# Optimization experiments

Hardware: AMD Instinct MI355X
Metric: run time of the kernel (lower is better)

## Reference

```python
import jax, jax.numpy as jnp
import numpy as np

N = 50000      # nodes
E = 800000     # edges (avg degree 16)
D_IN = 128     # node_feature_dim
H = 256        # hidden_dim
EPS = 1e-5     # BatchNorm eps


def setup_inputs() -> dict:
    key = jax.random.key(0)
    ks = jax.random.split(key, 32)
    inp = {
        "x": jax.random.normal(ks[0], (N, D_IN), jnp.float32),
        "edge_index": jax.random.randint(ks[1], (2, E), 0, N, jnp.int32),
    }
    dims = [(D_IN, H), (H, H), (H, H)]
    k = 2
    for i, (din, dout) in enumerate(dims):
        s = 1.0 / np.sqrt(din)
        inp[f"Wl{i}"] = jax.random.uniform(ks[k], (din, dout), jnp.float32, -s, s); k += 1
        inp[f"bl{i}"] = jax.random.uniform(ks[k], (dout,), jnp.float32, -s, s); k += 1
        inp[f"Wr{i}"] = jax.random.uniform(ks[k], (din, dout), jnp.float32, -s, s); k += 1
        inp[f"g{i}"] = jnp.ones((dout,), jnp.float32)
        inp[f"b{i}"] = jnp.zeros((dout,), jnp.float32)
        inp[f"rm{i}"] = jax.random.normal(ks[k], (dout,), jnp.float32) * 0.1; k += 1
        inp[f"rv{i}"] = jax.random.uniform(ks[k], (dout,), jnp.float32, 0.5, 1.5); k += 1
    return inp


def _sage(x, src, dst, Wl, bl, Wr):
    # PyG SAGEConv (aggr='mean'): out = lin_l(mean_{j in N(i)} x_j) + lin_r(x_i)
    deg = jax.ops.segment_sum(jnp.ones((src.shape[0],), x.dtype), dst, num_segments=N)
    agg = jax.ops.segment_sum(x[src], dst, num_segments=N)  # [N, d_in]
    mean = agg / jnp.maximum(deg, 1.0)[:, None]
    return mean @ Wl + bl + x @ Wr


def _bn(x, g, b, rm, rv):
    # eval-mode BatchNorm1d with running stats
    return (x - rm) * (g * jax.lax.rsqrt(rv + EPS)) + b


def reference(x, edge_index,
              Wl0, bl0, Wr0, g0, b0, rm0, rv0,
              Wl1, bl1, Wr1, g1, b1, rm1, rv1,
              Wl2, bl2, Wr2, g2, b2, rm2, rv2):
    src, dst = edge_index[0], edge_index[1]
    h = jax.nn.relu(_bn(_sage(x, src, dst, Wl0, bl0, Wr0), g0, b0, rm0, rv0))
    h = jax.nn.relu(_bn(_sage(h, src, dst, Wl1, bl1, Wr1), g1, b1, rm1, rv1))
    h = _bn(_sage(h, src, dst, Wl2, bl2, Wr2), g2, b2, rm2, rv2)
    return h  # [N, H] node embeddings (dropout is identity in eval mode)
```

## Files before the change

### kernel.cpp

```cpp
#include <hip/hip_runtime.h>
#include <hip/hip_bf16.h>

#define NNODES 50000
#define NEDGES 800000
#define HID 256
#define BN_EPS 1e-5f
#define SCAN_B ((NNODES + 255) / 256)

typedef __attribute__((ext_vector_type(8))) short short8v;
typedef __attribute__((ext_vector_type(4))) float f32x4;

__device__ inline void load_lds16(const void* g, void* l) {
    __builtin_amdgcn_global_load_lds(
        (const __attribute__((address_space(1))) unsigned int*)g,
        (__attribute__((address_space(3))) unsigned int*)l, 16, 0, 0);
}

__global__ void k_zero(int* p, int n) {
    int i = blockIdx.x * blockDim.x + threadIdx.x;
    if (i < n) p[i] = 0;
}

__global__ void k_countrank(const int* __restrict__ ei, int* __restrict__ cnt,
                            int* __restrict__ rank, int nE) {
    int e = blockIdx.x * blockDim.x + threadIdx.x;
    if (e < nE) rank[e] = atomicAdd(&cnt[ei[nE + e]], 1);
}

__global__ void k_bsum(const int* __restrict__ cnt, int* __restrict__ loc,
                       int* __restrict__ bsum, int n) {
    __shared__ int sh[256];
    int tid = threadIdx.x;
    int i = blockIdx.x * 256 + tid;
    int v = (i < n) ? cnt[i] : 0;
    sh[tid] = v;
    __syncthreads();
    for (int off = 1; off < 256; off <<= 1) {
        int t = (tid >= off) ? sh[tid - off] : 0;
        __syncthreads();
        sh[tid] += t;
        __syncthreads();
    }
    if (i < n) loc[i] = sh[tid] - v;
    if (tid == 255) bsum[blockIdx.x] = sh[255];
}

__global__ void k_bscan(int* __restrict__ bsum, int nb) {
    __shared__ int sh[256];
    int tid = threadIdx.x;
    int v = (tid < nb) ? bsum[tid] : 0;
    sh[tid] = v;
    __syncthreads();
    for (int off = 1; off < 256; off <<= 1) {
        int t = (tid >= off) ? sh[tid - off] : 0;
        __syncthreads();
        sh[tid] += t;
        __syncthreads();
    }
    if (tid < nb) bsum[tid] = sh[tid] - v;
}

__global__ void k_addoff(const int* __restrict__ loc, const int* __restrict__ bsum,
                         int* __restrict__ rowptr, int n, int nE) {
    int i = blockIdx.x * 256 + threadIdx.x;
    if (i < n) rowptr[i] = loc[i] + bsum[blockIdx.x];
    if (i == 0) rowptr[n] = nE;
}

__global__ void k_fill2(const int* __restrict__ ei, const int* __restrict__ rowptr,
                        const int* __restrict__ rank, int* __restrict__ col, int nE) {
    int e = blockIdx.x * blockDim.x + threadIdx.x;
    if (e < nE) col[rowptr[ei[nE + e]] + rank[e]] = ei[e];
}

__global__ void k_cast(const float* __restrict__ in, __hip_bfloat16* __restrict__ out, int n) {
    int i = blockIdx.x * blockDim.x + threadIdx.x;
    int base = i * 4;
    if (base + 3 < n) {
        float4 v = *(const float4*)(in + base);
        out[base + 0] = __float2bfloat16(v.x);
        out[base + 1] = __float2bfloat16(v.y);
        out[base + 2] = __float2bfloat16(v.z);
        out[base + 3] = __float2bfloat16(v.w);
    } else {
        for (int j = base; j < n; j++) out[j] = __float2bfloat16(in[j]);
    }
}

__global__ void k_transpose6(const float* __restrict__ s0, const float* __restrict__ s1,
                             const float* __restrict__ s2, const float* __restrict__ s3,
                             const float* __restrict__ s4, const float* __restrict__ s5,
                             __hip_bfloat16* __restrict__ d0, __hip_bfloat16* __restrict__ d1,
                             __hip_bfloat16* __restrict__ d2, __hip_bfloat16* __restrict__ d3,
                             __hip_bfloat16* __restrict__ d4, __hip_bfloat16* __restrict__ d5) {
    int f = blockIdx.x * blockDim.x + threadIdx.x;
    const float* src; __hip_bfloat16* dst; int K; int i;
    if (f < 65536) {
        K = 128;
        if (f < 32768) { src = s0; dst = d0; i = f; }
        else           { src = s1; dst = d1; i = f - 32768; }
    } else {
        K = 256;
        int r = f - 65536;
        int wsel = r >> 16;
        i = r & 65535;
        src = (wsel == 0) ? s2 : (wsel == 1) ? s3 : (wsel == 2) ? s4 : s5;
        dst = (wsel == 0) ? d2 : (wsel == 1) ? d3 : (wsel == 2) ? d4 : d5;
    }
    int k = i >> 8;
    int nn = i & 255;
    dst[nn * K + k] = __float2bfloat16(src[i]);
}

template <int D, int U>
__global__ void k_mean(const __hip_bfloat16* __restrict__ xin,
                       const int* __restrict__ rowptr, const int* __restrict__ col,
                       __hip_bfloat16* __restrict__ mean, int n) {
    constexpr int CPL = D / 8;
    constexpr int R = 64 / CPL;
    int gw = (blockIdx.x * blockDim.x + threadIdx.x) >> 6;
    int lane = threadIdx.x & 63;
    if (gw >= n) return;
    int beg = rowptr[gw], end = rowptr[gw + 1];
    int sub = lane / CPL;
    int fpos = lane % CPL;
    const uint4* base = (const uint4*)xin;

    float acc[8];
#pragma unroll
    for (int j = 0; j < 8; j++) acc[j] = 0.f;

    for (int p0 = beg; p0 < end; p0 += U * R) {
        int idx[U]; bool ok[U];
#pragma unroll
        for (int u = 0; u < U; u++) {
            int p = p0 + u * R + sub;
            ok[u] = (p < end);
            idx[u] = ok[u] ? col[p] : 0;
        }
        uint4 v[U];
#pragma unroll
        for (int u = 0; u < U; u++) {
            uint4 t = {0u, 0u, 0u, 0u};
            if (ok[u]) t = base[(size_t)idx[u] * CPL + fpos];
            v[u] = t;
        }
#pragma unroll
        for (int u = 0; u < U; u++) {
            const unsigned int uu[4] = {v[u].x, v[u].y, v[u].z, v[u].w};
#pragma unroll
            for (int j = 0; j < 4; j++) {
                acc[2 * j]     += __uint_as_float(uu[j] << 16);
                acc[2 * j + 1] += __uint_as_float(uu[j] & 0xffff0000u);
            }
        }
    }

    if constexpr (R >= 2) {
#pragma unroll
        for (int j = 0; j < 8; j++) acc[j] += __shfl_xor(acc[j], 32, 64);
    }
    if constexpr (R == 4) {
#pragma unroll
        for (int j = 0; j < 8; j++) acc[j] += __shfl_xor(acc[j], 16, 64);
    }

    if (sub == 0) {
        float inv = (end > beg) ? 1.f / (float)(end - beg) : 0.f;
        union { uint4 v; unsigned short s[8]; } o;
#pragma unroll
        for (int j = 0; j < 8; j++)
            o.s[j] = __bfloat16_as_ushort(__float2bfloat16(acc[j] * inv));
        *(uint4*)(mean + (size_t)gw * D + fpos * 8) = o.v;
    }
}

template <int K, typename OutT, int RELU>
__launch_bounds__(256)
__global__ void k_gemm(const __hip_bfloat16* __restrict__ A1,
                       const __hip_bfloat16* __restrict__ A2,
                       const __hip_bfloat16* __restrict__ W1t,
                       const __hip_bfloat16* __restrict__ W2t,
                       const float* __restrict__ bl,
                       const float* __restrict__ g,
                       const float* __restrict__ bb,
                       const float* __restrict__ rm,
                       const float* __restrict__ rv,
                       OutT* __restrict__ out, int n) {
    __shared__ __hip_bfloat16 As1[128 * 32];
    __shared__ __hip_bfloat16 As2[128 * 32];
    __shared__ __hip_bfloat16 Bs1[128 * 32];
    __shared__ __hip_bfloat16 Bs2[128 * 32];
    int tid = threadIdx.x;
    int lane = tid & 63;
    int w = tid >> 6;
    int quad = lane >> 4;
    int ml = lane & 15;
    int rowBase = (blockIdx.x >> 1) * 128;
    int colBase = (blockIdx.x & 1) * 128;
    int wr = w >> 1, wc = w & 1;

    f32x4 acc[4][4];
#pragma unroll
    for (int i = 0; i < 4; i++)
#pragma unroll
        for (int t = 0; t < 4; t++) acc[i][t] = {0.f, 0.f, 0.f, 0.f};

    int srow = tid >> 2;
    int sbyte = (tid & 3) * 16;

    for (int k0 = 0; k0 < K; k0 += 32) {
        __syncthreads();
#pragma unroll
        for (int h = 0; h < 2; h++) {
            int r = srow + h * 64;
            int grow = rowBase + r; if (grow >= n) grow = n - 1;
            int c = colBase + r;
            load_lds16((const char*)(A1 + (size_t)grow * K + k0) + sbyte,
                       (char*)As1 + r * 64 + sbyte);
            load_lds16((const char*)(A2 + (size_t)grow * K + k0) + sbyte,
                       (char*)As2 + r * 64 + sbyte);
            load_lds16((const char*)(W1t + (size_t)c * K + k0) + sbyte,
                       (char*)Bs1 + r * 64 + sbyte);
            load_lds16((const char*)(W2t + (size_t)c * K + k0) + sbyte,
                       (char*)Bs2 + r * 64 + sbyte);
        }
        __syncthreads();

        short8v af1[4], af2[4], bf1[4], bf2[4];
#pragma unroll
        for (int i = 0; i < 4; i++) {
            af1[i] = *(const short8v*)(As1 + (wr * 64 + i * 16 + ml) * 32 + quad * 8);
            af2[i] = *(const short8v*)(As2 + (wr * 64 + i * 16 + ml) * 32 + quad * 8);
        }
#pragma unroll
        for (int t = 0; t < 4; t++) {
            bf1[t] = *(const short8v*)(Bs1 + (wc * 64 + t * 16 + ml) * 32 + quad * 8);
            bf2[t] = *(const short8v*)(Bs2 + (wc * 64 + t * 16 + ml) * 32 + quad * 8);
        }
#pragma unroll
        for (int i = 0; i < 4; i++)
#pragma unroll
            for (int t = 0; t < 4; t++) {
                acc[i][t] = __builtin_amdgcn_mfma_f32_16x16x32_bf16(af1[i], bf1[t], acc[i][t], 0, 0, 0);
                acc[i][t] = __builtin_amdgcn_mfma_f32_16x16x32_bf16(af2[i], bf2[t], acc[i][t], 0, 0, 0);
            }
    }

#pragma unroll
    for (int t = 0; t < 4; t++) {
        int c = colBase + wc * 64 + t * 16 + ml;
        float sv = g[c] * rsqrtf(rv[c] + BN_EPS);
        float tv = (bl[c] - rm[c]) * sv + bb[c];
#pragma unroll
        for (int i = 0; i < 4; i++) {
            int row0 = rowBase + wr * 64 + i * 16 + quad * 4;
#pragma unroll
            for (int r = 0; r < 4; r++) {
                int row = row0 + r;
                if (row < n) {
                    float v = acc[i][t][r] * sv + tv;
                    if (RELU) v = fmaxf(v, 0.f);
                    if constexpr (sizeof(OutT) == 2)
                        out[(size_t)row * HID + c] = (OutT)__float2bfloat16(v);
                    else
                        out[(size_t)row * HID + c] = (OutT)v;
                }
            }
        }
    }
}

extern "C" void kernel_launch(void* const* d_in, const int* in_sizes, int n_in,
                              void* d_out, int out_size, void* d_ws, size_t ws_size,
                              hipStream_t stream) {
    const float* x = (const float*)d_in[0];
    const int* ei = (const int*)d_in[1];
    const float *Wl[3], *blv[3], *Wr[3], *g[3], *bb[3], *rm[3], *rv[3];
    for (int i = 0; i < 3; i++) {
        int b = 2 + i * 7;
        Wl[i]  = (const float*)d_in[b + 0];
        blv[i] = (const float*)d_in[b + 1];
        Wr[i]  = (const float*)d_in[b + 2];
        g[i]   = (const float*)d_in[b + 3];
        bb[i]  = (const float*)d_in[b + 4];
        rm[i]  = (const float*)d_in[b + 5];
        rv[i]  = (const float*)d_in[b + 6];
    }

    char* ob = (char*)d_out;
    __hip_bfloat16* xb = (__hip_bfloat16*)ob;
    __hip_bfloat16* h0 = (__hip_bfloat16*)(ob + (size_t)NNODES * 128 * 2);

    char* w = (char*)d_ws;
    size_t off = 0;
    auto alloc = [&](size_t bytes) {
        void* p = w + off;
        off += (bytes + 255) & ~(size_t)255;
        return p;
    };
    int* rowptr = (int*)alloc((NNODES + 1) * sizeof(int));
    int* cnt    = (int*)alloc(NNODES * sizeof(int));
    int* loc    = (int*)alloc(NNODES * sizeof(int));
    int* bsum   = (int*)alloc(SCAN_B * sizeof(int));
    int* rank   = (int*)alloc(NEDGES * sizeof(int));
    int* col    = (int*)alloc(NEDGES * sizeof(int));
    __hip_bfloat16* meanb = (__hip_bfloat16*)alloc((size_t)NNODES * HID * 2);
    __hip_bfloat16* h1    = (__hip_bfloat16*)alloc((size_t)NNODES * HID * 2);
    __hip_bfloat16* Wt[6];
    int Ks[6] = {128, 128, 256, 256, 256, 256};
    for (int i = 0; i < 6; i++) Wt[i] = (__hip_bfloat16*)alloc((size_t)Ks[i] * HID * 2);

    k_zero<<<SCAN_B, 256, 0, stream>>>(cnt, NNODES);
    k_countrank<<<(NEDGES + 255) / 256, 256, 0, stream>>>(ei, cnt, rank, NEDGES);
    k_bsum<<<SCAN_B, 256, 0, stream>>>(cnt, loc, bsum, NNODES);
    k_bscan<<<1, 256, 0, stream>>>(bsum, SCAN_B);
    k_addoff<<<SCAN_B, 256, 0, stream>>>(loc, bsum, rowptr, NNODES, NEDGES);
    k_fill2<<<(NEDGES + 255) / 256, 256, 0, stream>>>(ei, rowptr, rank, col, NEDGES);

    k_cast<<<(NNODES * 128 / 4 + 255) / 256, 256, 0, stream>>>(x, xb, NNODES * 128);

    k_transpose6<<<(327680 + 255) / 256, 256, 0, stream>>>(
        Wl[0], Wr[0], Wl[1], Wr[1], Wl[2], Wr[2],
        Wt[0], Wt[1], Wt[2], Wt[3], Wt[4], Wt[5]);

    int meanBlocks = (NNODES * 64 + 255) / 256;
    int gemmBlocks = ((NNODES + 127) / 128) * 2;

    k_mean<128, 4><<<meanBlocks, 256, 0, stream>>>(xb, rowptr, col, meanb, NNODES);
    k_gemm<128, __hip_bfloat16, 1><<<gemmBlocks, 256, 0, stream>>>(meanb, xb, Wt[0], Wt[1],
        blv[0], g[0], bb[0], rm[0], rv[0], h0, NNODES);

    k_mean<256, 8><<<meanBlocks, 256, 0, stream>>>(h0, rowptr, col, meanb, NNODES);
    k_gemm<256, __hip_bfloat16, 1><<<gemmBlocks, 256, 0, stream>>>(meanb, h0, Wt[2], Wt[3],
        blv[1], g[1], bb[1], rm[1], rv[1], h1, NNODES);

    k_mean<256, 8><<<meanBlocks, 256, 0, stream>>>(h1, rowptr, col, meanb, NNODES);
    k_gemm<256, float, 0><<<gemmBlocks, 256, 0, stream>>>(meanb, h1, Wt[4], Wt[5],
        blv[2], g[2], bb[2], rm[2], rv[2], (float*)d_out, NNODES);
}
```

Measured before the change: 419.4 us.

## Widen GEMM tile to full 256 columns and split mean aggregation into feature halves

The GEMM now has each block compute all 256 output columns for 128 rows, so each A tile is loaded once rather than by two column blocks. This doubles per-wave accumulators to 4x8 and sets launch bounds to two blocks per SM. The 256-wide mean aggregation is split into two launches, each gathering one 128-feature half with four edges in flight per wave. The aim is better cache locality on the gather, at the cost of re-reading the CSR indices twice. The larger B tile in LDS and the higher register pressure may reduce occupancy.

```diff
diff --git a/kernel.cpp b/kernel.cpp
--- a/kernel.cpp
+++ b/kernel.cpp
@@ -113,28 +113,28 @@
 }
 
 template <int D, int U>
-__global__ void k_mean(const __hip_bfloat16* __restrict__ xin,
-                       const int* __restrict__ rowptr, const int* __restrict__ col,
-                       __hip_bfloat16* __restrict__ mean, int n) {
-    constexpr int CPL = D / 8;
-    constexpr int R = 64 / CPL;
+__global__ void k_meanh(const __hip_bfloat16* __restrict__ xin,
+                        const int* __restrict__ rowptr, const int* __restrict__ col,
+                        __hip_bfloat16* __restrict__ mean, int n, int fo) {
+    constexpr int QPR = D / 8;
     int gw = (blockIdx.x * blockDim.x + threadIdx.x) >> 6;
     int lane = threadIdx.x & 63;
     if (gw >= n) return;
     int beg = rowptr[gw], end = rowptr[gw + 1];
-    int sub = lane / CPL;
-    int fpos = lane % CPL;
+    int sub = lane >> 4;
+    int fpos = lane & 15;
     const uint4* base = (const uint4*)xin;
+    int foq = fo >> 3;
 
     float acc[8];
 #pragma unroll
     for (int j = 0; j < 8; j++) acc[j] = 0.f;
 
-    for (int p0 = beg; p0 < end; p0 += U * R) {
+    for (int p0 = beg; p0 < end; p0 += U * 4) {
         int idx[U]; bool ok[U];
 #pragma unroll
         for (int u = 0; u < U; u++) {
-            int p = p0 + u * R + sub;
+            int p = p0 + u * 4 + sub;
             ok[u] = (p < end);
             idx[u] = ok[u] ? col[p] : 0;
         }
@@ -142,7 +142,7 @@
 #pragma unroll
         for (int u = 0; u < U; u++) {
             uint4 t = {0u, 0u, 0u, 0u};
-            if (ok[u]) t = base[(size_t)idx[u] * CPL + fpos];
+            if (ok[u]) t = base[(size_t)idx[u] * QPR + foq + fpos];
             v[u] = t;
         }
 #pragma unroll
@@ -156,14 +156,10 @@
         }
     }
 
-    if constexpr (R >= 2) {
-#pragma unroll
-        for (int j = 0; j < 8; j++) acc[j] += __shfl_xor(acc[j], 32, 64);
-    }
-    if constexpr (R == 4) {
-#pragma unroll
-        for (int j = 0; j < 8; j++) acc[j] += __shfl_xor(acc[j], 16, 64);
-    }
+#pragma unroll
+    for (int j = 0; j < 8; j++) acc[j] += __shfl_xor(acc[j], 32, 64);
+#pragma unroll
+    for (int j = 0; j < 8; j++) acc[j] += __shfl_xor(acc[j], 16, 64);
 
     if (sub == 0) {
         float inv = (end > beg) ? 1.f / (float)(end - beg) : 0.f;
@@ -171,40 +167,39 @@
 #pragma unroll
         for (int j = 0; j < 8; j++)
             o.s[j] = __bfloat16_as_ushort(__float2bfloat16(acc[j] * inv));
-        *(uint4*)(mean + (size_t)gw * D + fpos * 8) = o.v;
+        *(uint4*)(mean + (size_t)gw * D + fo + fpos * 8) = o.v;
     }
 }
 
 template <int K, typename OutT, int RELU>
-__launch_bounds__(256)
-__global__ void k_gemm(const __hip_bfloat16* __restrict__ A1,
-                       const __hip_bfloat16* __restrict__ A2,
-                       const __hip_bfloat16* __restrict__ W1t,
-                       const __hip_bfloat16* __restrict__ W2t,
-                       const float* __restrict__ bl,
-                       const float* __restrict__ g,
-                       const float* __restrict__ bb,
-                       const float* __restrict__ rm,
-                       const float* __restrict__ rv,
-                       OutT* __restrict__ out, int n) {
+__launch_bounds__(256, 2)
+__global__ void k_gemm2(const __hip_bfloat16* __restrict__ A1,
+                        const __hip_bfloat16* __restrict__ A2,
+                        const __hip_bfloat16* __restrict__ W1t,
+                        const __hip_bfloat16* __restrict__ W2t,
+                        const float* __restrict__ bl,
+                        const float* __restrict__ g,
+                        const float* __restrict__ bb,
+                        const float* __restrict__ rm,
+                        const float* __restrict__ rv,
+                        OutT* __restrict__ out, int n) {
     __shared__ __hip_bfloat16 As1[128 * 32];
     __shared__ __hip_bfloat16 As2[128 * 32];
-    __shared__ __hip_bfloat16 Bs1[128 * 32];
-    __shared__ __hip_bfloat16 Bs2[128 * 32];
+    __shared__ __hip_bfloat16 Bs1[256 * 32];
+    __shared__ __hip_bfloat16 Bs2[256 * 32];
     int tid = threadIdx.x;
     int lane = tid & 63;
     int w = tid >> 6;
     int quad = lane >> 4;
     int ml = lane & 15;
-    int rowBase = (blockIdx.x >> 1) * 128;
-    int colBase = (blockIdx.x & 1) * 128;
+    int rowBase = blockIdx.x * 128;
     int wr = w >> 1, wc = w & 1;
 
-    f32x4 acc[4][4];
+    f32x4 acc[4][8];
 #pragma unroll
     for (int i = 0; i < 4; i++)
 #pragma unroll
-        for (int t = 0; t < 4; t++) acc[i][t] = {0.f, 0.f, 0.f, 0.f};
+        for (int t = 0; t < 8; t++) acc[i][t] = {0.f, 0.f, 0.f, 0.f};
 
     int srow = tid >> 2;
     int sbyte = (tid & 3) * 16;
@@ -215,41 +210,42 @@
         for (int h = 0; h < 2; h++) {
             int r = srow + h * 64;
             int grow = rowBase + r; if (grow >= n) grow = n - 1;
-            int c = colBase + r;
             load_lds16((const char*)(A1 + (size_t)grow * K + k0) + sbyte,
                        (char*)As1 + r * 64 + sbyte);
             load_lds16((const char*)(A2 + (size_t)grow * K + k0) + sbyte,
                        (char*)As2 + r * 64 + sbyte);
+        }
+#pragma unroll
+        for (int h = 0; h < 4; h++) {
+            int c = srow + h * 64;
             load_lds16((const char*)(W1t + (size_t)c * K + k0) + sbyte,
-                       (char*)Bs1 + r * 64 + sbyte);
+                       (char*)Bs1 + c * 64 + sbyte);
             load_lds16((const char*)(W2t + (size_t)c * K + k0) + sbyte,
-                       (char*)Bs2 + r * 64 + sbyte);
-        }
-        __syncthreads();
-
-        short8v af1[4], af2[4], bf1[4], bf2[4];
+                       (char*)Bs2 + c * 64 + sbyte);
+        }
+        __syncthreads();
+
+        short8v af1[4], af2[4];
 #pragma unroll
         for (int i = 0; i < 4; i++) {
             af1[i] = *(const short8v*)(As1 + (wr * 64 + i * 16 + ml) * 32 + quad * 8);
             af2[i] = *(const short8v*)(As2 + (wr * 64 + i * 16 + ml) * 32 + quad * 8);
         }
 #pragma unroll
-        for (int t = 0; t < 4; t++) {
-            bf1[t] = *(const short8v*)(Bs1 + (wc * 64 + t * 16 + ml) * 32 + quad * 8);
-            bf2[t] = *(const short8v*)(Bs2 + (wc * 64 + t * 16 + ml) * 32 + quad * 8);
-        }
-#pragma unroll
-        for (int i = 0; i < 4; i++)
-#pragma unroll
-            for (int t = 0; t < 4; t++) {
-                acc[i][t] = __builtin_amdgcn_mfma_f32_16x16x32_bf16(af1[i], bf1[t], acc[i][t], 0, 0, 0);
-                acc[i][t] = __builtin_amdgcn_mfma_f32_16x16x32_bf16(af2[i], bf2[t], acc[i][t], 0, 0, 0);
+        for (int t = 0; t < 8; t++) {
+            short8v bf1 = *(const short8v*)(Bs1 + (wc * 128 + t * 16 + ml) * 32 + quad * 8);
+            short8v bf2 = *(const short8v*)(Bs2 + (wc * 128 + t * 16 + ml) * 32 + quad * 8);
+#pragma unroll
+            for (int i = 0; i < 4; i++) {
+                acc[i][t] = __builtin_amdgcn_mfma_f32_16x16x32_bf16(af1[i], bf1, acc[i][t], 0, 0, 0);
+                acc[i][t] = __builtin_amdgcn_mfma_f32_16x16x32_bf16(af2[i], bf2, acc[i][t], 0, 0, 0);
             }
-    }
-
-#pragma unroll
-    for (int t = 0; t < 4; t++) {
-        int c = colBase + wc * 64 + t * 16 + ml;
+        }
+    }
+
+#pragma unroll
+    for (int t = 0; t < 8; t++) {
+        int c = wc * 128 + t * 16 + ml;
         float sv = g[c] * rsqrtf(rv[c] + BN_EPS);
         float tv = (bl[c] - rm[c]) * sv + bb[c];
 #pragma unroll
@@ -325,17 +321,19 @@
         Wt[0], Wt[1], Wt[2], Wt[3], Wt[4], Wt[5]);
 
     int meanBlocks = (NNODES * 64 + 255) / 256;
-    int gemmBlocks = ((NNODES + 127) / 128) * 2;
-
-    k_mean<128, 4><<<meanBlocks, 256, 0, stream>>>(xb, rowptr, col, meanb, NNODES);
-    k_gemm<128, __hip_bfloat16, 1><<<gemmBlocks, 256, 0, stream>>>(meanb, xb, Wt[0], Wt[1],
+    int gemmBlocks = (NNODES + 127) / 128;
+
+    k_meanh<128, 4><<<meanBlocks, 256, 0, stream>>>(xb, rowptr, col, meanb, NNODES, 0);
+    k_gemm2<128, __hip_bfloat16, 1><<<gemmBlocks, 256, 0, stream>>>(meanb, xb, Wt[0], Wt[1],
         blv[0], g[0], bb[0], rm[0], rv[0], h0, NNODES);
 
-    k_mean<256, 8><<<meanBlocks, 256, 0, stream>>>(h0, rowptr, col, meanb, NNODES);
-    k_gemm<256, __hip_bfloat16, 1><<<gemmBlocks, 256, 0, stream>>>(meanb, h0, Wt[2], Wt[3],
+    k_meanh<256, 4><<<meanBlocks, 256, 0, stream>>>(h0, rowptr, col, meanb, NNODES, 0);
+    k_meanh<256, 4><<<meanBlocks, 256, 0, stream>>>(h0, rowptr, col, meanb, NNODES, 128);
+    k_gemm2<256, __hip_bfloat16, 1><<<gemmBlocks, 256, 0, stream>>>(meanb, h0, Wt[2], Wt[3],
         blv[1], g[1], bb[1], rm[1], rv[1], h1, NNODES);
 
-    k_mean<256, 8><<<meanBlocks, 256, 0, stream>>>(h1, rowptr, col, meanb, NNODES);
-    k_gemm<256, float, 0><<<gemmBlocks, 256, 0, stream>>>(meanb, h1, Wt[4], Wt[5],
+    k_meanh<256, 4><<<meanBlocks, 256, 0, stream>>>(h1, rowptr, col, meanb, NNODES, 0);
+    k_meanh<256, 4><<<meanBlocks, 256, 0, stream>>>(h1, rowptr, col, meanb, NNODES, 128);
+    k_gemm2<256, float, 0><<<gemmBlocks, 256, 0, stream>>>(meanb, h1, Wt[4], Wt[5],
         blv[2], g[2], bb[2], rm[2], rv[2], (float*)d_out, NNODES);
 }
```

Result: no change. 411.2 us (-2.0%).
